# Optimization experiments

Hardware: AMD Instinct MI355X
Metric: run time of the kernel (lower is better)

The kernel has to match this reference:

```python
import jax, jax.numpy as jnp
import numpy as np

B, S, D, H = 8, 1024, 768, 12
C = D // H  # head dim = 64
NEG_SLOPE = 0.2  # PyG GATConv default leaky_relu slope


def setup_inputs() -> dict:
    key = jax.random.key(0)
    ks = jax.random.split(key, 12)
    s = 0.02
    return {
        "hidden_states": jax.random.normal(ks[0], (B, S, D), jnp.float32),
        "transformer_output": jax.random.normal(ks[1], (B, S, D), jnp.float32),
        # GATConv params: lin (no bias), att_src/att_dst [H, C], bias [H*C]
        "W_gat": jax.random.normal(ks[2], (D, D), jnp.float32) * s,
        "att_src": jax.random.normal(ks[3], (H, C), jnp.float32) * s,
        "att_dst": jax.random.normal(ks[4], (H, C), jnp.float32) * s,
        "b_gat": jnp.zeros((D,), jnp.float32),
        # gat_projection
        "W_proj": jax.random.normal(ks[5], (D, D), jnp.float32) * s,
        "b_proj": jnp.zeros((D,), jnp.float32),
        # fusion
        "W_fus": jax.random.normal(ks[6], (2 * D, D), jnp.float32) * s,
        "b_fus": jnp.zeros((D,), jnp.float32),
    }


def reference(hidden_states, transformer_output, W_gat, att_src, att_dst,
              b_gat, W_proj, b_proj, W_fus, b_fus):
    # --- GATConv on a fully-connected graph (+ default self-loops) ---
    # Fully connected + self loops => softmax over ALL sources per target,
    # so the scatter-softmax reduces to dense attention.
    x = (hidden_states @ W_gat).reshape(B, S, H, C)          # [B,S,H,C]
    a_src = jnp.einsum('bshc,hc->bhs', x, att_src)           # score contribution of source j
    a_dst = jnp.einsum('bshc,hc->bhs', x, att_dst)           # score contribution of target i
    # scores[b,h,i,j] = a_dst_i + a_src_j, then leaky_relu, softmax over j
    scores = jax.nn.leaky_relu(a_dst[:, :, :, None] + a_src[:, :, None, :],
                               negative_slope=NEG_SLOPE)     # [B,H,S,S]
    attn = jax.nn.softmax(scores, axis=-1)
    out = jnp.einsum('bhij,bjhc->bihc', attn, x)             # aggregate sources
    gat_out = out.reshape(B, S, D) + b_gat                   # concat heads + bias

    # --- projection, fusion ---
    graph_output = gat_out @ W_proj + b_proj
    fused = jnp.concatenate([transformer_output, graph_output], axis=-1)
    fused = fused @ W_fus + b_fus
    return fused
```

## Files before the change

### kernel.cpp

```cpp
#include <hip/hip_runtime.h>
#include <hip/hip_bf16.h>

#define NB 8
#define NS 1024
#define ND 768
#define NH 12
#define NC 64
#define NEG 0.2f
#define NBUK 128

typedef __attribute__((ext_vector_type(8))) short bf16x8;
typedef __attribute__((ext_vector_type(4))) float f32x4;

static __device__ __forceinline__ float bf2f(unsigned short u) {
    union { float f; unsigned int i; } v; v.i = ((unsigned int)u) << 16; return v.f;
}
static __device__ __forceinline__ unsigned short f2bf(float f) {
    union { float f; unsigned int i; } v; v.f = f;
    unsigned int r = v.i + 0x7FFFu + ((v.i >> 16) & 1u);
    return (unsigned short)(r >> 16);
}

static __device__ __forceinline__ void gload16(const unsigned short* g, unsigned short* l) {
    __builtin_amdgcn_global_load_lds((const __attribute__((address_space(1))) void*)g,
                                     (__attribute__((address_space(3))) void*)l, 16, 0, 0);
}

static __device__ __forceinline__ int swz_bid(int orig, int nwg) {
    int q = nwg >> 3, r = nwg & 7;
    int xcd = orig & 7, idx = orig >> 3;
    return (xcd < r ? xcd * (q + 1) : r * (q + 1) + (xcd - r) * q) + idx;
}

__global__ __launch_bounds__(256) void k_prep(const float* __restrict__ hs, const float* __restrict__ to,
                                              const float* __restrict__ Wp, const float* __restrict__ Wg,
                                              const float* __restrict__ Wf, const float* __restrict__ bp,
                                              const float* __restrict__ bfu,
                                              unsigned short* __restrict__ h_bf, unsigned short* __restrict__ t_bf,
                                              unsigned short* __restrict__ Wp_bf, unsigned short* __restrict__ WgT,
                                              unsigned short* __restrict__ WfT, float* __restrict__ bias_tot,
                                              int n1, int n2) {
    const int NT1 = (ND / 32) * (3 * ND / 32);
    const int NT2 = (ND * 8) / 256;
    int blk = blockIdx.x, t = threadIdx.x;
    if (blk < NT1) {
        __shared__ float tile[32][33];
        int bx = blk % (ND / 32), by = blk / (ND / 32);
        const float* src; unsigned short* dst; int K, k0;
        if (by < ND / 32) { src = Wg; dst = WgT; K = ND; k0 = by * 32; }
        else { src = Wf; dst = WfT; K = 2 * ND; k0 = (by - ND / 32) * 32; }
        int n0 = bx * 32;
        int r = t >> 3, c4 = (t & 7) * 4;
        float4 v = *reinterpret_cast<const float4*>(src + (size_t)(k0 + r) * ND + n0 + c4);
        tile[r][c4] = v.x; tile[r][c4 + 1] = v.y; tile[r][c4 + 2] = v.z; tile[r][c4 + 3] = v.w;
        __syncthreads();
        ushort4 o;
        o.x = f2bf(tile[c4][r]); o.y = f2bf(tile[c4 + 1][r]);
        o.z = f2bf(tile[c4 + 2][r]); o.w = f2bf(tile[c4 + 3][r]);
        *reinterpret_cast<ushort4*>(dst + (size_t)(n0 + r) * K + k0 + c4) = o;
    } else if (blk < NT1 + NT2) {
        int gid = (blk - NT1) * 256 + t;
        int c = gid >> 3, sl = gid & 7;
        float acc = 0.f;
        int k0 = sl * 96;
#pragma unroll 8
        for (int k = k0; k < k0 + 96; k++) acc += bp[k] * Wf[(size_t)(ND + k) * ND + c];
        acc += __shfl_down(acc, 1, 64);
        acc += __shfl_down(acc, 2, 64);
        acc += __shfl_down(acc, 4, 64);
        if (sl == 0) bias_tot[c] = acc + bfu[c];
    } else {
        int gid = (blk - NT1 - NT2) * 256 + t;
        const float* s; unsigned short* d; int i;
        if (gid < n1) { s = hs; d = h_bf; i = gid; }
        else if (gid < 2 * n1) { s = to; d = t_bf; i = gid - n1; }
        else { s = Wp; d = Wp_bf; i = gid - 2 * n1; if (i >= n2) return; }
        i *= 4;
        float4 v = *reinterpret_cast<const float4*>(s + i);
        ushort4 o;
        o.x = f2bf(v.x); o.y = f2bf(v.y); o.z = f2bf(v.z); o.w = f2bf(v.w);
        *reinterpret_cast<ushort4*>(d + i) = o;
    }
}

__global__ __launch_bounds__(256) void k_bucket(const float* __restrict__ a_src,
                                                float4* __restrict__ pack,
                                                int* __restrict__ bstart,
                                                float* __restrict__ smax_g,
                                                float2* __restrict__ bparam,
                                                float* __restrict__ zb) {
    int bh = blockIdx.x, t = threadIdx.x;
    __shared__ float v[1024];
    __shared__ int bi[1024];
    __shared__ float red[256];
    __shared__ int cnt[NBUK], pre[NBUK];
    __shared__ float zs1[NBUK], zs2[NBUK];
    for (int i = t; i < 1024; i += 256) v[i] = a_src[(size_t)bh * 1024 + i];
    if (t < NBUK) { cnt[t] = 0; zs1[t] = 0.f; zs2[t] = 0.f; }
    __syncthreads();
    float lm = -1e30f, ln = 1e30f;
    for (int i = t; i < 1024; i += 256) { lm = fmaxf(lm, v[i]); ln = fminf(ln, v[i]); }
    red[t] = lm; __syncthreads();
    for (int s = 128; s > 0; s >>= 1) { if (t < s) red[t] = fmaxf(red[t], red[t + s]); __syncthreads(); }
    float mx = red[0]; __syncthreads();
    red[t] = ln; __syncthreads();
    for (int s = 128; s > 0; s >>= 1) { if (t < s) red[t] = fminf(red[t], red[t + s]); __syncthreads(); }
    float mn = red[0]; __syncthreads();
    float scale = (float)NBUK / fmaxf(mx - mn, 1e-20f);
    for (int i = t; i < 1024; i += 256) {
        int bk = (int)((v[i] - mn) * scale);
        bk = min(max(bk, 0), NBUK - 1);
        bi[i] = bk;
        atomicAdd(&cnt[bk], 1);
    }
    __syncthreads();
    if (t < NBUK) pre[t] = cnt[t];
    __syncthreads();
    for (int off = 1; off < NBUK; off <<= 1) {
        int x = (t >= off && t < NBUK) ? pre[t - off] : 0;
        __syncthreads();
        if (t < NBUK) pre[t] += x;
        __syncthreads();
    }
    if (t < NBUK) {
        int start = pre[t] - cnt[t];
        bstart[bh * (NBUK + 1) + t] = start;
        cnt[t] = start;
    }
    if (t == 0) {
        bstart[bh * (NBUK + 1) + NBUK] = 1024;
        smax_g[bh] = mx;
        bparam[bh] = make_float2(mn, scale);
    }
    __syncthreads();
    for (int i = t; i < 1024; i += 256) {
        int pos = atomicAdd(&cnt[bi[i]], 1);
        float u = v[i] - mx;
        float4 p;
        p.x = u; p.y = __expf(u); p.z = __expf(0.2f * u); p.w = __int_as_float(i);
        pack[(size_t)bh * 1024 + pos] = p;
        atomicAdd(&zs1[bi[i]], p.y);
        atomicAdd(&zs2[bi[i]], p.z);
    }
    __syncthreads();
    for (int off = 1; off < NBUK; off <<= 1) {
        float x1 = (t >= off && t < NBUK) ? zs1[t - off] : 0.f;
        float x2 = (t >= off && t < NBUK) ? zs2[t - off] : 0.f;
        __syncthreads();
        if (t < NBUK) { zs1[t] += x1; zs2[t] += x2; }
        __syncthreads();
    }
    if (t < NBUK) {
        zb[(size_t)(bh * NBUK + t) * 2] = zs1[t];
        zb[(size_t)(bh * NBUK + t) * 2 + 1] = zs2[t];
    }
}

__global__ __launch_bounds__(256) void k_bsum(const unsigned short* __restrict__ x_bf,
                                              const float4* __restrict__ pack,
                                              const int* __restrict__ bstart,
                                              float* __restrict__ P) {
    int grp = blockIdx.x, bh = blockIdx.y;
    int t = threadIdx.x, w = t >> 6, lane = t & 63;
    int b = bh / NH, h = bh % NH;
    const float4* pk = pack + (size_t)bh * 1024;
    const unsigned short* xb = x_bf + (size_t)b * NS * ND + h * 64 + lane;
#pragma unroll
    for (int r = 0; r < 2; r++) {
        int bk = grp * 8 + w * 2 + r;
        int ks = bstart[bh * (NBUK + 1) + bk], ke = bstart[bh * (NBUK + 1) + bk + 1];
        float V1p0 = 0.f, V1p1 = 0.f, V1p2 = 0.f, V1p3 = 0.f;
        float V2p0 = 0.f, V2p1 = 0.f, V2p2 = 0.f, V2p3 = 0.f;
        int k = ks;
        for (; k + 4 <= ke; k += 4) {
            float4 p0 = pk[k], p1 = pk[k + 1], p2 = pk[k + 2], p3 = pk[k + 3];
            float x0 = bf2f(xb[(size_t)__float_as_int(p0.w) * ND]);
            float x1 = bf2f(xb[(size_t)__float_as_int(p1.w) * ND]);
            float x2 = bf2f(xb[(size_t)__float_as_int(p2.w) * ND]);
            float x3 = bf2f(xb[(size_t)__float_as_int(p3.w) * ND]);
            V1p0 = fmaf(p0.y, x0, V1p0); V2p0 = fmaf(p0.z, x0, V2p0);
            V1p1 = fmaf(p1.y, x1, V1p1); V2p1 = fmaf(p1.z, x1, V2p1);
            V1p2 = fmaf(p2.y, x2, V1p2); V2p2 = fmaf(p2.z, x2, V2p2);
            V1p3 = fmaf(p3.y, x3, V1p3); V2p3 = fmaf(p3.z, x3, V2p3);
        }
        for (; k < ke; k++) {
            float4 p = pk[k];
            float xv = bf2f(xb[(size_t)__float_as_int(p.w) * ND]);
            V1p0 = fmaf(p.y, xv, V1p0); V2p0 = fmaf(p.z, xv, V2p0);
        }
        float V1 = (V1p0 + V1p1) + (V1p2 + V1p3);
        float V2 = (V2p0 + V2p1) + (V2p2 + V2p3);
        size_t o = ((size_t)(bh * NBUK + bk) * 2) * 64 + lane;
        P[o] = V1; P[o + 64] = V2;
    }
}

__global__ __launch_bounds__(256) void k_bpref(float* __restrict__ P) {
    int bh = blockIdx.x, t = threadIdx.x, w = t >> 6, lane = t & 63;
    __shared__ float segV[4][2][64];
    size_t base = (size_t)bh * NBUK;
    float V1 = 0.f, V2 = 0.f;
    for (int g = 0; g < 4; ++g) {
        float a1[8], a2[8];
#pragma unroll
        for (int r = 0; r < 8; r++) {
            size_t o = ((base + w * 32 + g * 8 + r) * 2) * 64 + lane;
            a1[r] = P[o]; a2[r] = P[o + 64];
        }
#pragma unroll
        for (int r = 0; r < 8; r++) { V1 += a1[r]; a1[r] = V1; V2 += a2[r]; a2[r] = V2; }
#pragma unroll
        for (int r = 0; r < 8; r++) {
            size_t o = ((base + w * 32 + g * 8 + r) * 2) * 64 + lane;
            P[o] = a1[r]; P[o + 64] = a2[r];
        }
    }
    segV[w][0][lane] = V1; segV[w][1][lane] = V2;
    __syncthreads();
    if (w > 0) {
        float O1 = 0.f, O2 = 0.f;
        for (int w2 = 0; w2 < w; w2++) { O1 += segV[w2][0][lane]; O2 += segV[w2][1][lane]; }
        for (int g = 0; g < 4; ++g) {
            float a1[8], a2[8];
#pragma unroll
            for (int r = 0; r < 8; r++) {
                size_t o = ((base + w * 32 + g * 8 + r) * 2) * 64 + lane;
                a1[r] = P[o]; a2[r] = P[o + 64];
            }
#pragma unroll
            for (int r = 0; r < 8; r++) {
                size_t o = ((base + w * 32 + g * 8 + r) * 2) * 64 + lane;
                P[o] = a1[r] + O1; P[o + 64] = a2[r] + O2;
            }
        }
    }
}

__global__ __launch_bounds__(256) void k_apply3(const float* __restrict__ P,
                                                const float* __restrict__ zb,
                                                const float* __restrict__ a_dst,
                                                const float* __restrict__ smax_g,
                                                const float2* __restrict__ bparam,
                                                const float* __restrict__ b_gat,
                                                unsigned short* __restrict__ gat) {
    int bh = blockIdx.y, t = threadIdx.x, w = t >> 6, lane = t & 63;
    int b = bh / NH, h = bh % NH;
    float sm = smax_g[bh];
    float2 bp_ = bparam[bh];
    float mn = bp_.x, scale = bp_.y;
    size_t pb = (size_t)bh * NBUK;
    float T1 = P[((pb + NBUK - 1) * 2) * 64 + lane];
    float z1tot = zb[(pb + NBUK - 1) * 2];
    float bias = b_gat[h * 64 + lane];
#pragma unroll
    for (int q = 0; q < 8; q++) {
        int i = blockIdx.x * 32 + w * 8 + q;
        float d = a_dst[(size_t)bh * 1024 + i];
        float dm = d + sm;
        float m = dm > 0.f ? dm : NEG * dm;
        float c1 = __expf(dm - m);
        float c2 = __expf(NEG * dm - m);
        int e = (int)floorf((-d - mn) * scale + 0.5f);
        e = min(max(e, 0), NBUK);
        float P1f = 0.f, P2f = 0.f, z1f = 0.f, z2f = 0.f;
        if (e > 0) {
            size_t o = ((pb + e - 1) * 2) * 64 + lane;
            P1f = P[o]; P2f = P[o + 64];
            z1f = zb[(pb + e - 1) * 2];
            z2f = zb[(pb + e - 1) * 2 + 1];
        }
        float num = c1 * (T1 - P1f) + c2 * P2f;
        float Z = c1 * (z1tot - z1f) + c2 * z2f;
        gat[((size_t)(b * NS + i)) * ND + h * 64 + lane] = f2bf(num / Z + bias);
    }
}

template <bool OUT_BF16, bool BIAS, bool DUAL, bool ATT>
static __device__ __forceinline__ void gemm_body(
    const unsigned short* __restrict__ A1, const unsigned short* __restrict__ B1,
    int lda1, int ldb1,
    const unsigned short* __restrict__ A2, const unsigned short* __restrict__ B2,
    int lda2, int ldb2,
    const float* __restrict__ bias, void* __restrict__ Cout,
    int m0, int n0, int N, int K,
    unsigned short* sA, unsigned short* sB,
    const float* __restrict__ att_src, const float* __restrict__ att_dst,
    float* __restrict__ a_src, float* __restrict__ a_dst) {
    int t = threadIdx.x, wave = t >> 6, lane = t & 63;
    int lr = lane & 15, kq = lane >> 4;
    int srow = t >> 3;
    int scol = ((t & 7) ^ (srow & 7)) * 8;
    int cs0 = ((kq) ^ (lr & 7)) * 8;
    int cs1 = ((4 + kq) ^ (lr & 7)) * 8;
    const int kh = K >> 6;
    const int nsteps = (DUAL ? 2 : 1) * kh;
    f32x4 acc[4][2] = {};

    auto STAGE = [&](int s, int buf) {
        const unsigned short* A; const unsigned short* Bt; int lda, ldb, k0;
        if (DUAL && s >= kh) { A = A2; Bt = B2; lda = lda2; ldb = ldb2; k0 = (s - kh) << 6; }
        else { A = A1; Bt = B1; lda = lda1; ldb = ldb1; k0 = s << 6; }
        const unsigned short* gA = A + (size_t)(m0 + srow) * lda + scol + k0;
        const unsigned short* gB = Bt + (size_t)(n0 + srow) * ldb + scol + k0;
        unsigned short* dA = sA + buf * 4096 + t * 8;
        unsigned short* dB = sB + buf * 8192 + t * 8;
        gload16(gA, dA);
        gload16(gA + (size_t)32 * lda, dA + 2048);
        gload16(gB, dB);
        gload16(gB + (size_t)32 * ldb, dB + 2048);
        gload16(gB + (size_t)64 * ldb, dB + 4096);
        gload16(gB + (size_t)96 * ldb, dB + 6144);
    };
    auto COMPUTE = [&](int cur) {
        unsigned short* cA = sA + cur * 4096;
        unsigned short* cB = sB + cur * 8192;
        bf16x8 a0[4], a1v[4], b0[2], b1v[2];
#pragma unroll
        for (int m = 0; m < 4; m++) {
            a0[m]  = *reinterpret_cast<bf16x8*>(&cA[(m * 16 + lr) * 64 + cs0]);
            a1v[m] = *reinterpret_cast<bf16x8*>(&cA[(m * 16 + lr) * 64 + cs1]);
        }
#pragma unroll
        for (int n = 0; n < 2; n++) {
            b0[n]  = *reinterpret_cast<bf16x8*>(&cB[(wave * 32 + n * 16 + lr) * 64 + cs0]);
            b1v[n] = *reinterpret_cast<bf16x8*>(&cB[(wave * 32 + n * 16 + lr) * 64 + cs1]);
        }
#pragma unroll
        for (int m = 0; m < 4; m++)
#pragma unroll
            for (int n = 0; n < 2; n++) {
                acc[m][n] = __builtin_amdgcn_mfma_f32_16x16x32_bf16(a0[m], b0[n], acc[m][n], 0, 0, 0);
                acc[m][n] = __builtin_amdgcn_mfma_f32_16x16x32_bf16(a1v[m], b1v[n], acc[m][n], 0, 0, 0);
            }
    };

    STAGE(0, 0);
    STAGE(1, 1);
    for (int s = 0; s < nsteps - 1; s++) {
        int cur = s & 1;
        asm volatile("s_waitcnt vmcnt(6)" ::: "memory");
        __builtin_amdgcn_s_barrier();
        __builtin_amdgcn_sched_barrier(0);
        COMPUTE(cur);
        __builtin_amdgcn_sched_barrier(0);
        __builtin_amdgcn_s_barrier();
        if (s + 2 < nsteps) STAGE(s + 2, cur);
    }
    asm volatile("s_waitcnt vmcnt(0)" ::: "memory");
    __builtin_amdgcn_s_barrier();
    __builtin_amdgcn_sched_barrier(0);
    COMPUTE((nsteps - 1) & 1);

    int rg = kq * 4;
#pragma unroll
    for (int m = 0; m < 4; m++) {
#pragma unroll
        for (int n = 0; n < 2; n++) {
            int col = n0 + wave * 32 + n * 16 + lr;
            float bv = BIAS ? bias[col] : 0.0f;
#pragma unroll
            for (int r = 0; r < 4; r++) {
                int row = m0 + m * 16 + rg + r;
                float v = acc[m][n][r] + bv;
                if (OUT_BF16) {
                    ((unsigned short*)Cout)[(size_t)row * N + col] = f2bf(v);
                } else {
                    ((float*)Cout)[(size_t)row * N + col] = v;
                }
            }
        }
    }

    if (ATT) {
        __syncthreads();
        float ds_[4][4] = {}, dd_[4][4] = {};
#pragma unroll
        for (int n = 0; n < 2; n++) {
            int colg = n0 + wave * 32 + n * 16 + lr;
            float as_v = att_src[colg];
            float ad_v = att_dst[colg];
#pragma unroll
            for (int m = 0; m < 4; m++)
#pragma unroll
                for (int r = 0; r < 4; r++) {
                    ds_[m][r] = fmaf(acc[m][n][r], as_v, ds_[m][r]);
                    dd_[m][r] = fmaf(acc[m][n][r], ad_v, dd_[m][r]);
                }
        }
#pragma unroll
        for (int off = 1; off <= 8; off <<= 1)
#pragma unroll
            for (int m = 0; m < 4; m++)
#pragma unroll
                for (int r = 0; r < 4; r++) {
                    ds_[m][r] += __shfl_xor(ds_[m][r], off, 64);
                    dd_[m][r] += __shfl_xor(dd_[m][r], off, 64);
                }
        float* red = (float*)sA;
        if (lr == 0) {
#pragma unroll
            for (int m = 0; m < 4; m++)
#pragma unroll
                for (int r = 0; r < 4; r++) {
                    int rl = m * 16 + kq * 4 + r;
                    red[wave * 64 + rl] = ds_[m][r];
                    red[256 + wave * 64 + rl] = dd_[m][r];
                }
        }
        __syncthreads();
        if (t < 128) {
            int hb = t >> 6, rl = t & 63;
            float vs = red[(hb * 2) * 64 + rl] + red[(hb * 2 + 1) * 64 + rl];
            float vd = red[256 + (hb * 2) * 64 + rl] + red[256 + (hb * 2 + 1) * 64 + rl];
            int grow = m0 + rl;
            int b = grow >> 10, sdx = grow & 1023;
            int head = (n0 >> 6) + hb;
            a_src[((size_t)b * NH + head) * NS + sdx] = vs;
            a_dst[((size_t)b * NH + head) * NS + sdx] = vd;
        }
    }
}

__global__ __launch_bounds__(256) void k_gemm_pair(
    const unsigned short* __restrict__ Aa, const unsigned short* __restrict__ Ba,
    unsigned short* __restrict__ Ca, int NBna, int Na, int Ka, int lda_a, int ldb_a, int nwg_a,
    const unsigned short* __restrict__ Ab, const unsigned short* __restrict__ Bb,
    unsigned short* __restrict__ Cb, int NBnb, int Nb, int Kb, int lda_b, int ldb_b,
    const float* __restrict__ att_src, const float* __restrict__ att_dst,
    float* __restrict__ a_src, float* __restrict__ a_dst) {
    __shared__ alignas(16) unsigned short sA[2 * 64 * 64];
    __shared__ alignas(16) unsigned short sB[2 * 128 * 64];
    int wg = swz_bid(blockIdx.x, gridDim.x);
    if (wg < nwg_a) {
        gemm_body<true, false, false, true>(Aa, Ba, lda_a, ldb_a, nullptr, nullptr, 0, 0, nullptr,
                                            Ca, (wg / NBna) * 64, (wg % NBna) * 128, Na, Ka, sA, sB,
                                            att_src, att_dst, a_src, a_dst);
    } else {
        wg -= nwg_a;
        gemm_body<true, false, false, false>(Ab, Bb, lda_b, ldb_b, nullptr, nullptr, 0, 0, nullptr,
                                             Cb, (wg / NBnb) * 64, (wg % NBnb) * 128, Nb, Kb, sA, sB,
                                             nullptr, nullptr, nullptr, nullptr);
    }
}

__global__ __launch_bounds__(256) void k_gemm_dual(
    const unsigned short* __restrict__ A1, const unsigned short* __restrict__ B1,
    const unsigned short* __restrict__ A2, const unsigned short* __restrict__ B2,
    const float* __restrict__ bias, float* __restrict__ out,
    int NBn, int N, int K, int lda, int ldb1, int ldb2) {
    __shared__ alignas(16) unsigned short sA[2 * 64 * 64];
    __shared__ alignas(16) unsigned short sB[2 * 128 * 64];
    int wg = swz_bid(blockIdx.x, gridDim.x);
    gemm_body<false, true, true, false>(A1, B1, lda, ldb1, A2, B2, lda, ldb2, bias,
                                        out, (wg / NBn) * 64, (wg % NBn) * 128, N, K, sA, sB,
                                        nullptr, nullptr, nullptr, nullptr);
}

extern "C" void kernel_launch(void* const* d_in, const int* in_sizes, int n_in,
                              void* d_out, int out_size, void* d_ws, size_t ws_size,
                              hipStream_t stream) {
    const float* hs  = (const float*)d_in[0];
    const float* to  = (const float*)d_in[1];
    const float* Wg  = (const float*)d_in[2];
    const float* asv = (const float*)d_in[3];
    const float* adv = (const float*)d_in[4];
    const float* bg  = (const float*)d_in[5];
    const float* Wp  = (const float*)d_in[6];
    const float* bp  = (const float*)d_in[7];
    const float* Wf  = (const float*)d_in[8];
    const float* bfu = (const float*)d_in[9];
    float* out = (float*)d_out;

    char* ws = (char*)d_ws;
    size_t off = 0;
    auto alloc = [&](size_t bytes) -> void* {
        void* p = ws + off;
        off = (off + bytes + 255) & ~(size_t)255;
        return p;
    };
    const size_t NBSD = (size_t)NB * NS * ND;
    const int NBH = NB * NH;
    unsigned short* h_bf   = (unsigned short*)alloc(NBSD * 2);
    unsigned short* x_bf   = (unsigned short*)alloc(NBSD * 2);
    unsigned short* t_bf   = (unsigned short*)alloc(NBSD * 2);
    unsigned short* WgT    = (unsigned short*)alloc((size_t)ND * ND * 2);
    unsigned short* Wp_bf  = (unsigned short*)alloc((size_t)ND * ND * 2);
    unsigned short* WfT    = (unsigned short*)alloc((size_t)2 * ND * ND * 2);
    unsigned short* WcombT = (unsigned short*)alloc((size_t)ND * ND * 2);
    float*  bias_tot = (float*)alloc((size_t)ND * 4);
    float*  a_src = (float*)alloc((size_t)NBH * NS * 4);
    float*  a_dst = (float*)alloc((size_t)NBH * NS * 4);
    float4* pack  = (float4*)alloc((size_t)NBH * NS * 16);
    int*    bstart = (int*)alloc((size_t)NBH * (NBUK + 1) * 4);
    float*  P     = (float*)alloc((size_t)NBH * NBUK * 2 * 64 * 4);
    float*  zb    = (float*)alloc((size_t)NBH * NBUK * 2 * 4);
    float*  smaxb = (float*)alloc((size_t)NBH * 4);
    float2* bparam = (float2*)alloc((size_t)NBH * 8);

    int n1 = (int)NBSD / 4, n2 = ND * ND / 4;
    const int NT1 = (ND / 32) * (3 * ND / 32);
    const int NT2 = (ND * 8) / 256;
    const int NT3 = (2 * n1 + n2 + 255) / 256;
    k_prep<<<NT1 + NT2 + NT3, 256, 0, stream>>>(hs, to, Wp, Wg, Wf, bp, bfu,
                                                h_bf, t_bf, Wp_bf, WgT, WfT, bias_tot, n1, n2);

    int nwg1 = (NB * NS / 64) * (ND / 128);
    int nwgW = (ND / 64) * (ND / 128);
    k_gemm_pair<<<nwg1 + nwgW, 256, 0, stream>>>(
        h_bf, WgT, x_bf, ND / 128, ND, ND, ND, ND, nwg1,
        WfT + ND, Wp_bf, WcombT, ND / 128, ND, ND, 2 * ND, ND,
        asv, adv, a_src, a_dst);

    k_bucket<<<NBH, 256, 0, stream>>>(a_src, pack, bstart, smaxb, bparam, zb);
    k_bsum<<<dim3(NBUK / 8, NBH), 256, 0, stream>>>(x_bf, pack, bstart, P);
    k_bpref<<<NBH, 256, 0, stream>>>(P);

    unsigned short* gat_bf = h_bf;
    k_apply3<<<dim3(NS / 32, NBH), 256, 0, stream>>>(P, zb, a_dst, smaxb, bparam, bg, gat_bf);

    k_gemm_dual<<<(NB * NS / 64) * (ND / 128), 256, 0, stream>>>(
        t_bf, WfT, gat_bf, WcombT, bias_tot, out, ND / 128, ND, ND, ND, 2 * ND, ND);
}
```

Measured before the change: 118.0 us.

## Enlarge GEMM tiles to 128x128 with 2x2 wave layout and per-wave head reduction

The GEMM block tile grows from 64x128 to 128x128, with the four waves arranged 2x2 so each wave computes a 64x64 sub-tile (4x4 MFMA accumulators). This raises per-wave register and LDS reuse and halves the number of workgroups. Because each wave now owns a full 64-column head, the attention-score reduction is done inside the wave and written directly to global memory, which drops the LDS cross-wave reduction and its two syncthreads. The trade-off is more accumulator registers, double the LDS for A, and fewer workgroups (384 for the main GEMMs), which may reduce occupancy and leave CUs underfilled.

Measured after the change: 111.5 us, median of 2. -5.5%, faster.

```diff
diff --git a/kernel.cpp b/kernel.cpp
--- a/kernel.cpp
+++ b/kernel.cpp
@@ -287,6 +287,7 @@
     const float* __restrict__ att_src, const float* __restrict__ att_dst,
     float* __restrict__ a_src, float* __restrict__ a_dst) {
     int t = threadIdx.x, wave = t >> 6, lane = t & 63;
+    int wm = wave >> 1, wn = wave & 1;
     int lr = lane & 15, kq = lane >> 4;
     int srow = t >> 3;
     int scol = ((t & 7) ^ (srow & 7)) * 8;
@@ -294,7 +295,7 @@
     int cs1 = ((4 + kq) ^ (lr & 7)) * 8;
     const int kh = K >> 6;
     const int nsteps = (DUAL ? 2 : 1) * kh;
-    f32x4 acc[4][2] = {};
+    f32x4 acc[4][4] = {};
 
     auto STAGE = [&](int s, int buf) {
         const unsigned short* A; const unsigned short* Bt; int lda, ldb, k0;
@@ -302,33 +303,32 @@
         else { A = A1; Bt = B1; lda = lda1; ldb = ldb1; k0 = s << 6; }
         const unsigned short* gA = A + (size_t)(m0 + srow) * lda + scol + k0;
         const unsigned short* gB = Bt + (size_t)(n0 + srow) * ldb + scol + k0;
-        unsigned short* dA = sA + buf * 4096 + t * 8;
+        unsigned short* dA = sA + buf * 8192 + t * 8;
         unsigned short* dB = sB + buf * 8192 + t * 8;
-        gload16(gA, dA);
-        gload16(gA + (size_t)32 * lda, dA + 2048);
-        gload16(gB, dB);
-        gload16(gB + (size_t)32 * ldb, dB + 2048);
-        gload16(gB + (size_t)64 * ldb, dB + 4096);
-        gload16(gB + (size_t)96 * ldb, dB + 6144);
+#pragma unroll
+        for (int p = 0; p < 4; p++) {
+            gload16(gA + (size_t)(p * 32) * lda, dA + p * 2048);
+            gload16(gB + (size_t)(p * 32) * ldb, dB + p * 2048);
+        }
     };
     auto COMPUTE = [&](int cur) {
-        unsigned short* cA = sA + cur * 4096;
+        unsigned short* cA = sA + cur * 8192;
         unsigned short* cB = sB + cur * 8192;
-        bf16x8 a0[4], a1v[4], b0[2], b1v[2];
+        bf16x8 a0[4], a1v[4], b0[4], b1v[4];
 #pragma unroll
         for (int m = 0; m < 4; m++) {
-            a0[m]  = *reinterpret_cast<bf16x8*>(&cA[(m * 16 + lr) * 64 + cs0]);
-            a1v[m] = *reinterpret_cast<bf16x8*>(&cA[(m * 16 + lr) * 64 + cs1]);
-        }
-#pragma unroll
-        for (int n = 0; n < 2; n++) {
-            b0[n]  = *reinterpret_cast<bf16x8*>(&cB[(wave * 32 + n * 16 + lr) * 64 + cs0]);
-            b1v[n] = *reinterpret_cast<bf16x8*>(&cB[(wave * 32 + n * 16 + lr) * 64 + cs1]);
+            a0[m]  = *reinterpret_cast<bf16x8*>(&cA[(wm * 64 + m * 16 + lr) * 64 + cs0]);
+            a1v[m] = *reinterpret_cast<bf16x8*>(&cA[(wm * 64 + m * 16 + lr) * 64 + cs1]);
+        }
+#pragma unroll
+        for (int n = 0; n < 4; n++) {
+            b0[n]  = *reinterpret_cast<bf16x8*>(&cB[(wn * 64 + n * 16 + lr) * 64 + cs0]);
+            b1v[n] = *reinterpret_cast<bf16x8*>(&cB[(wn * 64 + n * 16 + lr) * 64 + cs1]);
         }
 #pragma unroll
         for (int m = 0; m < 4; m++)
 #pragma unroll
-            for (int n = 0; n < 2; n++) {
+            for (int n = 0; n < 4; n++) {
                 acc[m][n] = __builtin_amdgcn_mfma_f32_16x16x32_bf16(a0[m], b0[n], acc[m][n], 0, 0, 0);
                 acc[m][n] = __builtin_amdgcn_mfma_f32_16x16x32_bf16(a1v[m], b1v[n], acc[m][n], 0, 0, 0);
             }
@@ -338,7 +338,7 @@
     STAGE(1, 1);
     for (int s = 0; s < nsteps - 1; s++) {
         int cur = s & 1;
-        asm volatile("s_waitcnt vmcnt(6)" ::: "memory");
+        asm volatile("s_waitcnt vmcnt(8)" ::: "memory");
         __builtin_amdgcn_s_barrier();
         __builtin_amdgcn_sched_barrier(0);
         COMPUTE(cur);
@@ -355,12 +355,12 @@
 #pragma unroll
     for (int m = 0; m < 4; m++) {
 #pragma unroll
-        for (int n = 0; n < 2; n++) {
-            int col = n0 + wave * 32 + n * 16 + lr;
+        for (int n = 0; n < 4; n++) {
+            int col = n0 + wn * 64 + n * 16 + lr;
             float bv = BIAS ? bias[col] : 0.0f;
 #pragma unroll
             for (int r = 0; r < 4; r++) {
-                int row = m0 + m * 16 + rg + r;
+                int row = m0 + wm * 64 + m * 16 + rg + r;
                 float v = acc[m][n][r] + bv;
                 if (OUT_BF16) {
                     ((unsigned short*)Cout)[(size_t)row * N + col] = f2bf(v);
@@ -372,11 +372,11 @@
     }
 
     if (ATT) {
-        __syncthreads();
+        int head = (n0 >> 6) + wn;
         float ds_[4][4] = {}, dd_[4][4] = {};
 #pragma unroll
-        for (int n = 0; n < 2; n++) {
-            int colg = n0 + wave * 32 + n * 16 + lr;
+        for (int n = 0; n < 4; n++) {
+            int colg = head * 64 + n * 16 + lr;
             float as_v = att_src[colg];
             float ad_v = att_dst[colg];
 #pragma unroll
@@ -396,27 +396,16 @@
                     ds_[m][r] += __shfl_xor(ds_[m][r], off, 64);
                     dd_[m][r] += __shfl_xor(dd_[m][r], off, 64);
                 }
-        float* red = (float*)sA;
         if (lr == 0) {
 #pragma unroll
             for (int m = 0; m < 4; m++)
 #pragma unroll
                 for (int r = 0; r < 4; r++) {
-                    int rl = m * 16 + kq * 4 + r;
-                    red[wave * 64 + rl] = ds_[m][r];
-                    red[256 + wave * 64 + rl] = dd_[m][r];
+                    int grow = m0 + wm * 64 + m * 16 + kq * 4 + r;
+                    int b = grow >> 10, sdx = grow & 1023;
+                    a_src[((size_t)b * NH + head) * NS + sdx] = ds_[m][r];
+                    a_dst[((size_t)b * NH + head) * NS + sdx] = dd_[m][r];
                 }
-        }
-        __syncthreads();
-        if (t < 128) {
-            int hb = t >> 6, rl = t & 63;
-            float vs = red[(hb * 2) * 64 + rl] + red[(hb * 2 + 1) * 64 + rl];
-            float vd = red[256 + (hb * 2) * 64 + rl] + red[256 + (hb * 2 + 1) * 64 + rl];
-            int grow = m0 + rl;
-            int b = grow >> 10, sdx = grow & 1023;
-            int head = (n0 >> 6) + hb;
-            a_src[((size_t)b * NH + head) * NS + sdx] = vs;
-            a_dst[((size_t)b * NH + head) * NS + sdx] = vd;
         }
     }
 }
@@ -428,17 +417,17 @@
     unsigned short* __restrict__ Cb, int NBnb, int Nb, int Kb, int lda_b, int ldb_b,
     const float* __restrict__ att_src, const float* __restrict__ att_dst,
     float* __restrict__ a_src, float* __restrict__ a_dst) {
-    __shared__ alignas(16) unsigned short sA[2 * 64 * 64];
+    __shared__ alignas(16) unsigned short sA[2 * 128 * 64];
     __shared__ alignas(16) unsigned short sB[2 * 128 * 64];
     int wg = swz_bid(blockIdx.x, gridDim.x);
     if (wg < nwg_a) {
         gemm_body<true, false, false, true>(Aa, Ba, lda_a, ldb_a, nullptr, nullptr, 0, 0, nullptr,
-                                            Ca, (wg / NBna) * 64, (wg % NBna) * 128, Na, Ka, sA, sB,
+                                            Ca, (wg / NBna) * 128, (wg % NBna) * 128, Na, Ka, sA, sB,
                                             att_src, att_dst, a_src, a_dst);
     } else {
         wg -= nwg_a;
         gemm_body<true, false, false, false>(Ab, Bb, lda_b, ldb_b, nullptr, nullptr, 0, 0, nullptr,
-                                             Cb, (wg / NBnb) * 64, (wg % NBnb) * 128, Nb, Kb, sA, sB,
+                                             Cb, (wg / NBnb) * 128, (wg % NBnb) * 128, Nb, Kb, sA, sB,
                                              nullptr, nullptr, nullptr, nullptr);
     }
 }
@@ -448,11 +437,11 @@
     const unsigned short* __restrict__ A2, const unsigned short* __restrict__ B2,
     const float* __restrict__ bias, float* __restrict__ out,
     int NBn, int N, int K, int lda, int ldb1, int ldb2) {
-    __shared__ alignas(16) unsigned short sA[2 * 64 * 64];
+    __shared__ alignas(16) unsigned short sA[2 * 128 * 64];
     __shared__ alignas(16) unsigned short sB[2 * 128 * 64];
     int wg = swz_bid(blockIdx.x, gridDim.x);
     gemm_body<false, true, true, false>(A1, B1, lda, ldb1, A2, B2, lda, ldb2, bias,
-                                        out, (wg / NBn) * 64, (wg % NBn) * 128, N, K, sA, sB,
+                                        out, (wg / NBn) * 128, (wg % NBn) * 128, N, K, sA, sB,
                                         nullptr, nullptr, nullptr, nullptr);
 }
 
@@ -504,8 +493,8 @@
     k_prep<<<NT1 + NT2 + NT3, 256, 0, stream>>>(hs, to, Wp, Wg, Wf, bp, bfu,
                                                 h_bf, t_bf, Wp_bf, WgT, WfT, bias_tot, n1, n2);
 
-    int nwg1 = (NB * NS / 64) * (ND / 128);
-    int nwgW = (ND / 64) * (ND / 128);
+    int nwg1 = (NB * NS / 128) * (ND / 128);
+    int nwgW = (ND / 128) * (ND / 128);
     k_gemm_pair<<<nwg1 + nwgW, 256, 0, stream>>>(
         h_bf, WgT, x_bf, ND / 128, ND, ND, ND, ND, nwg1,
         WfT + ND, Wp_bf, WcombT, ND / 128, ND, ND, 2 * ND, ND,
@@ -518,6 +507,6 @@
     unsigned short* gat_bf = h_bf;
     k_apply3<<<dim3(NS / 32, NBH), 256, 0, stream>>>(P, zb, a_dst, smaxb, bparam, bg, gat_bf);
 
-    k_gemm_dual<<<(NB * NS / 64) * (ND / 128), 256, 0, stream>>>(
+    k_gemm_dual<<<(NB * NS / 128) * (ND / 128), 256, 0, stream>>>(
         t_bf, WfT, gat_bf, WcombT, bias_tot, out, ND / 128, ND, ND, ND, 2 * ND, ND);
 }
```
